# Kernel tuning notes

Hardware: AMD Instinct MI355X
Metric: run time of the kernel (lower is better)

Reference implementation:

```python
import jax, jax.numpy as jnp
import numpy as np

B, NE, NR, D1, D2, L = 64, 40000, 500, 200, 200, 64
BN_EPS = 1e-5


def _batchnorm(x, gamma, beta):
    # training-mode BatchNorm1d: biased batch statistics over axis 0
    mu = jnp.mean(x, axis=0)
    var = jnp.var(x, axis=0)
    return gamma * (x - mu) * jax.lax.rsqrt(var + BN_EPS) + beta


def setup_inputs() -> dict:
    key = jax.random.key(0)
    ks = jax.random.split(key, 10)
    return {
        "e1_idx": jax.random.randint(ks[0], (B,), 0, NE),
        "r_idx": jax.random.randint(ks[1], (B,), 0, NR),
        "E": jax.random.normal(ks[2], (NE, D1), dtype=jnp.float32),
        "R": jax.random.normal(ks[3], (NR, D2), dtype=jnp.float32),
        # W ~ Uniform(-1, 1) as in the torch module
        "W": jax.random.uniform(ks[4], (D2, D1, D1), dtype=jnp.float32, minval=-1.0, maxval=1.0),
        # literals normalized into [0, 1]
        "lits": jax.random.uniform(ks[5], (NE, L), dtype=jnp.float32),
        "c": jax.random.normal(ks[6], (L,), dtype=jnp.float32) * 0.1,
        # variance buffer must be positive
        "var_l": jax.random.uniform(ks[7], (L,), dtype=jnp.float32, minval=0.5, maxval=1.5),
        "nf": jax.random.normal(ks[8], (NR, L), dtype=jnp.float32) * 0.1,
        "bn0_gamma": jnp.ones((D1,), jnp.float32),
        "bn0_beta": jnp.zeros((D1,), jnp.float32),
        "bn1_gamma": jnp.ones((D1,), jnp.float32),
        "bn1_beta": jnp.zeros((D1,), jnp.float32),
    }


def reference(e1_idx, r_idx, E, R, W, lits, c, var_l, nf,
              bn0_gamma, bn0_beta, bn1_gamma, bn1_beta):
    # --- TuckER core ---
    e1 = E[e1_idx]                                   # (B, d1)
    x = _batchnorm(e1, bn0_gamma, bn0_beta)          # (B, d1)
    r = R[r_idx]                                     # (B, d2)
    W_mat = jnp.einsum('bk,kij->bij', r, W)          # (B, d1, d1)
    x = jnp.einsum('bi,bij->bj', x, W_mat)           # (B, d1)
    x = _batchnorm(x, bn1_gamma, bn1_beta)
    score_l = x @ E.T                                # (B, N)

    # --- KBLN numeric-literal branch ---
    n_h = lits[e1_idx]                               # (B, L)
    # broadcast instead of .repeat: (B, 1, L) - (1, N, L) -> (B, N, L)
    n = n_h[:, None, :] - lits[None, :, :]
    phi = jnp.exp(-jnp.square(n - c) / var_l)        # (B, N, L)
    w_nf = nf[r_idx]                                 # (B, L)
    score_n = jnp.einsum('bnl,bl->bn', phi, w_nf)    # (B, N)

    return jax.nn.sigmoid(score_l + score_n)
```

## Files before the change

kernel.cpp:

```cpp
#include <hip/hip_runtime.h>
#include <math.h>

#define BB    64
#define NEC   40000
#define NRC   500
#define D1C   200
#define D2C   200
#define LLC   64
#define BN_EPS 1e-5f
#define LOG2E 1.4426950408889634f

#define WS_XT    0
#define WS_RT    12800
#define WS_TAP   25600
#define WS_WP    29696
#define WS_SL    33792
#define WS_X2BH  33856
#define WS_X2BL  42048
#define WS_Y     50240

typedef short s8v __attribute__((ext_vector_type(8)));
typedef float f4v __attribute__((ext_vector_type(4)));

__device__ __forceinline__ unsigned short bf16_rne(float x) {
  unsigned b = __float_as_uint(x);
  unsigned r = b + 0x7FFFu + ((b >> 16) & 1u);
  return (unsigned short)(r >> 16);
}
__device__ __forceinline__ void split2(float x, unsigned short& h,
                                       unsigned short& l) {
  h = bf16_rne(x);
  float hf = __uint_as_float(((unsigned)h) << 16);
  l = bf16_rne(x - hf);
}

__global__ __launch_bounds__(256) void prep_kernel(
    const int* __restrict__ e1_idx, const int* __restrict__ r_idx,
    const float* __restrict__ E, const float* __restrict__ R,
    const float* __restrict__ lits, const float* __restrict__ c,
    const float* __restrict__ var_l, const float* __restrict__ nf,
    const float* __restrict__ bn0g, const float* __restrict__ bn0b,
    float* __restrict__ ws) {
  float* xT  = ws + WS_XT;
  float* rT  = ws + WS_RT;
  float* taP = ws + WS_TAP;
  float* wP  = ws + WS_WP;
  float* sl  = ws + WS_SL;
  int tid = threadIdx.x;

  if (blockIdx.x == 0) {
    if (tid < D1C) {
      int j = tid;
      float sum = 0.f, sq = 0.f;
      for (int b = 0; b < BB; b++) {
        float e = E[e1_idx[b] * D1C + j];
        sum += e; sq += e * e;
      }
      float mean = sum * (1.f / 64.f);
      float var  = sq  * (1.f / 64.f) - mean * mean;
      float inv  = __builtin_amdgcn_rsqf(var + BN_EPS);
      float g    = bn0g[j] * inv;
      float be   = bn0b[j] - mean * g;
      for (int b = 0; b < BB; b++) {
        xT[j * 64 + b] = g * E[e1_idx[b] * D1C + j] + be;
      }
    }
  } else if (blockIdx.x == 1) {
    for (int idx = tid; idx < D2C * 64; idx += 256) {
      int k = idx >> 6, b = idx & 63;
      rT[idx] = R[r_idx[b] * D2C + k];
    }
  } else if (blockIdx.x == 2) {
    for (int idx = tid; idx < LLC * 64; idx += 256) {
      int l = idx >> 6, b = idx & 63;
      float s = sqrtf(LOG2E / var_l[l]);
      float a = (lits[e1_idx[b] * LLC + l] - c[l]) * s;
      int bp = (b & 15) * 4 + (b >> 4);
      taP[l * 64 + bp] = a + a;
      wP[l * 64 + bp]  = nf[r_idx[b] * LLC + l] * __builtin_amdgcn_exp2f(-a * a);
    }
    if (tid < LLC) sl[tid] = sqrtf(LOG2E / var_l[tid]);
  } else {
    unsigned* z = (unsigned*)(ws + WS_X2BH);
    for (int i = tid; i < 16384; i += 256) z[i] = 0u;
  }
}

__global__ __launch_bounds__(128) void stage1_kernel(
    const float* __restrict__ W, const float* __restrict__ ws_in,
    float* __restrict__ y) {
  const float* xT = ws_in + WS_XT;
  const float* rT = ws_in + WS_RT;
  int k = blockIdx.x, jq = blockIdx.y;
  int lane = threadIdx.x & 63;
  int wid = __builtin_amdgcn_readfirstlane(threadIdx.x >> 6);
  int j0 = jq * 20 + wid * 10;

  float r = rT[k * 64 + lane];
  float acc[10];
#pragma unroll
  for (int jj = 0; jj < 10; jj++) acc[jj] = 0.f;

  const float* Wk = W + (k * D1C) * D1C + j0;
  for (int i = 0; i < D1C; i++) {
    float xv = xT[i * 64 + lane];
    const float* wr = Wk + i * D1C;
#pragma unroll
    for (int jj = 0; jj < 10; jj++) acc[jj] += xv * wr[jj];
  }

  float* yo = y + (k * D1C + j0) * 64 + lane;
#pragma unroll
  for (int jj = 0; jj < 10; jj++) yo[jj * 64] = r * acc[jj];
}

__global__ __launch_bounds__(256) void reduce_bn1_kernel(
    const float* __restrict__ y, const float* __restrict__ bn1g,
    const float* __restrict__ bn1b, float* __restrict__ ws) {
  int j = blockIdx.x;
  int tid = threadIdx.x, b = tid & 63, kq = tid >> 6;

  float s = 0.f;
  const float* yp = y + (kq * 50 * D1C + j) * 64 + b;
  for (int k = 0; k < 50; k++) s += yp[k * D1C * 64];

  __shared__ float part[256];
  part[tid] = s;
  __syncthreads();
  if (tid < 64) {
    float v = part[tid] + part[64 + tid] + part[128 + tid] + part[192 + tid];
    float sum = v, sq = v * v;
#pragma unroll
    for (int o = 32; o > 0; o >>= 1) {
      sum += __shfl_xor(sum, o, 64);
      sq  += __shfl_xor(sq,  o, 64);
    }
    float mean = sum * (1.f / 64.f);
    float var  = sq  * (1.f / 64.f) - mean * mean;
    float inv  = __builtin_amdgcn_rsqf(var + BN_EPS);
    float g    = bn1g[j] * inv;
    float be   = bn1b[j] - mean * g;
    float xv   = g * v + be;
    unsigned short h, l;
    split2(xv, h, l);
    unsigned short* xh = (unsigned short*)(ws + WS_X2BH);
    unsigned short* xl = (unsigned short*)(ws + WS_X2BL);
    xh[tid * 256 + j] = h;
    xl[tid * 256 + j] = l;
  }
}

__global__ __launch_bounds__(256, 2) void final_kernel(
    const float* __restrict__ E, const float* __restrict__ lits,
    const float* __restrict__ ws, float* __restrict__ out) {
  const float* taP = ws + WS_TAP;
  const float* wP  = ws + WS_WP;
  const float* sl  = ws + WS_SL;
  const unsigned short* x2bh = (const unsigned short*)(ws + WS_X2BH);
  const unsigned short* x2bl = (const unsigned short*)(ws + WS_X2BL);

  __shared__ float SM[9216];
  unsigned short* Ah = (unsigned short*)SM;
  unsigned short* Al = Ah + 4608;
  unsigned short* Bh = Ah + 9216;
  unsigned short* Bl = Ah + 13824;

  int n0 = blockIdx.x * 64;
  int tid = threadIdx.x;
  int lane = tid & 63;
  int w = __builtin_amdgcn_readfirstlane(tid >> 6);
  int ln = lane & 15;
  int quad = lane >> 4;

  f4v acc[4];
#pragma unroll
  for (int t = 0; t < 4; t++) acc[t] = (f4v){0.f, 0.f, 0.f, 0.f};

  for (int q = 0; q < 4; q++) {
    int k0 = q * 64;
    __syncthreads();
#pragma unroll
    for (int it = 0; it < 4; it++) {
      int idx = tid + it * 256;
      int row = idx >> 4, c4 = idx & 15, cc = c4 * 4;
      float4 v = make_float4(0.f, 0.f, 0.f, 0.f);
      if (k0 + cc < 200) v = *(const float4*)(E + (n0 + row) * D1C + k0 + cc);
      unsigned short h0, l0, h1, l1, h2, l2, h3, l3;
      split2(v.x, h0, l0); split2(v.y, h1, l1);
      split2(v.z, h2, l2); split2(v.w, h3, l3);
      *(ushort4*)(Ah + row * 72 + cc) = make_ushort4(h0, h1, h2, h3);
      *(ushort4*)(Al + row * 72 + cc) = make_ushort4(l0, l1, l2, l3);
    }
#pragma unroll
    for (int it = 0; it < 4; it++) {
      int idx = tid + it * 256;
      int row = idx >> 4, c4 = idx & 15;
      *(ushort4*)(Bh + row * 72 + c4 * 4) =
          *(const ushort4*)(x2bh + row * 256 + k0 + c4 * 4);
      *(ushort4*)(Bl + row * 72 + c4 * 4) =
          *(const ushort4*)(x2bl + row * 256 + k0 + c4 * 4);
    }
    __syncthreads();

    const unsigned short* Ab  = Ah + (16 * w + ln) * 72 + quad * 8;
    const unsigned short* Alb = Al + (16 * w + ln) * 72 + quad * 8;
#pragma unroll
    for (int ks = 0; ks < 64; ks += 32) {
      s8v ah = *(const s8v*)(Ab + ks);
      s8v al = *(const s8v*)(Alb + ks);
#pragma unroll
      for (int t = 0; t < 4; t++) {
        s8v bh = *(const s8v*)(Bh + (16 * t + ln) * 72 + quad * 8 + ks);
        s8v bl = *(const s8v*)(Bl + (16 * t + ln) * 72 + quad * 8 + ks);
        acc[t] = __builtin_amdgcn_mfma_f32_16x16x32_bf16(ah, bh, acc[t], 0, 0, 0);
        acc[t] = __builtin_amdgcn_mfma_f32_16x16x32_bf16(al, bh, acc[t], 0, 0, 0);
        acc[t] = __builtin_amdgcn_mfma_f32_16x16x32_bf16(ah, bl, acc[t], 0, 0, 0);
      }
    }
  }

  float* Llds = SM;
  float* TAl  = SM + 4352;
  float* Wl   = SM + 6400;
  int nlb = 16 * w + 4 * quad;

  __syncthreads();
#pragma unroll
  for (int it = 0; it < 4; it++) {
    int idx = tid + it * 256;
    int row = idx >> 4, c4 = idx & 15;
    float4 v = *(const float4*)(lits + (n0 + row) * LLC + c4 * 4);
    int l = c4 * 4;
    Llds[(l + 0) * 68 + row] = v.x * sl[l + 0];
    Llds[(l + 1) * 68 + row] = v.y * sl[l + 1];
    Llds[(l + 2) * 68 + row] = v.z * sl[l + 2];
    Llds[(l + 3) * 68 + row] = v.w * sl[l + 3];
  }

  for (int h = 0; h < 2; h++) {
    __syncthreads();
#pragma unroll
    for (int it = 0; it < 2; it++) {
      int idx = tid + it * 256;
      ((float4*)TAl)[idx] = ((const float4*)(taP + h * 2048))[idx];
      ((float4*)Wl)[idx]  = ((const float4*)(wP  + h * 2048))[idx];
    }
    __syncthreads();
    for (int ll = 0; ll < 32; ll++) {
      float4 Lv = *(const float4*)(Llds + (h * 32 + ll) * 68 + nlb);
      float4 ta = *(const float4*)(TAl + ll * 64 + 4 * ln);
      float4 wv = *(const float4*)(Wl  + ll * 64 + 4 * ln);
      float Lc[4]  = {Lv.x, Lv.y, Lv.z, Lv.w};
      float tac[4] = {ta.x, ta.y, ta.z, ta.w};
      float wvc[4] = {wv.x, wv.y, wv.z, wv.w};
      float n2[4];
#pragma unroll
      for (int r = 0; r < 4; r++) n2[r] = -Lc[r] * Lc[r];
#pragma unroll
      for (int t = 0; t < 4; t++) {
#pragma unroll
        for (int r = 0; r < 4; r++) {
          acc[t][r] += wvc[t] *
              __builtin_amdgcn_exp2f(__builtin_fmaf(tac[t], Lc[r], n2[r]));
        }
      }
    }
  }

#pragma unroll
  for (int t = 0; t < 4; t++) {
    float4 o;
    o.x = __builtin_amdgcn_rcpf(1.f + __builtin_amdgcn_exp2f(-LOG2E * acc[t][0]));
    o.y = __builtin_amdgcn_rcpf(1.f + __builtin_amdgcn_exp2f(-LOG2E * acc[t][1]));
    o.z = __builtin_amdgcn_rcpf(1.f + __builtin_amdgcn_exp2f(-LOG2E * acc[t][2]));
    o.w = __builtin_amdgcn_rcpf(1.f + __builtin_amdgcn_exp2f(-LOG2E * acc[t][3]));
    *(float4*)(out + (size_t)(16 * t + ln) * NEC + n0 + nlb) = o;
  }
}

extern "C" void kernel_launch(void* const* d_in, const int* in_sizes, int n_in,
                              void* d_out, int out_size, void* d_ws, size_t ws_size,
                              hipStream_t stream) {
  (void)in_sizes; (void)n_in; (void)out_size; (void)ws_size;
  const int*   e1    = (const int*)d_in[0];
  const int*   ri    = (const int*)d_in[1];
  const float* E     = (const float*)d_in[2];
  const float* R     = (const float*)d_in[3];
  const float* W     = (const float*)d_in[4];
  const float* lits  = (const float*)d_in[5];
  const float* c     = (const float*)d_in[6];
  const float* var_l = (const float*)d_in[7];
  const float* nf    = (const float*)d_in[8];
  const float* bn0g  = (const float*)d_in[9];
  const float* bn0b  = (const float*)d_in[10];
  const float* bn1g  = (const float*)d_in[11];
  const float* bn1b  = (const float*)d_in[12];
  float* out = (float*)d_out;
  float* ws  = (float*)d_ws;
  float* y   = ws + WS_Y;

  prep_kernel<<<4, 256, 0, stream>>>(e1, ri, E, R, lits, c, var_l, nf,
                                     bn0g, bn0b, ws);
  stage1_kernel<<<dim3(200, 10), 128, 0, stream>>>(W, ws, y);
  reduce_bn1_kernel<<<200, 256, 0, stream>>>(y, bn1g, bn1b, ws);
  final_kernel<<<625, 256, 0, stream>>>(E, lits, ws, out);
}
```

Before: 205.8 us.

## Restructure stage1 as register-tiled GEMM with async global-to-LDS double buffering

```diff
diff --git a/kernel.cpp b/kernel.cpp
--- a/kernel.cpp
+++ b/kernel.cpp
@@ -32,6 +32,12 @@
   h = bf16_rne(x);
   float hf = __uint_as_float(((unsigned)h) << 16);
   l = bf16_rne(x - hf);
+}
+
+typedef __attribute__((address_space(1))) const void gvoid_t;
+typedef __attribute__((address_space(3))) void lvoid_t;
+__device__ __forceinline__ void gload_lds16(const float* g, float* l) {
+  __builtin_amdgcn_global_load_lds((gvoid_t*)g, (lvoid_t*)l, 16, 0, 0);
 }
 
 __global__ __launch_bounds__(256) void prep_kernel(
@@ -86,32 +92,79 @@
   }
 }
 
-__global__ __launch_bounds__(128) void stage1_kernel(
+#define S1_STAGE(buf_, s_) do {                                         \
+    int gbase_ = kbase + (s_) * 8000;                                   \
+    _Pragma("unroll")                                                   \
+    for (int r_ = 0; r_ < 4; r_++) {                                    \
+      int off_ = r_ * 2048 + w * 256;                                   \
+      int gi_ = gbase_ + off_ + lane4;                                  \
+      gi_ = gi_ < 7999996 ? gi_ : 7999996;                              \
+      gload_lds16(W + gi_, &Wb[buf_][off_]);                            \
+    }                                                                   \
+  } while (0)
+
+__global__ __launch_bounds__(512) void stage1_kernel(
     const float* __restrict__ W, const float* __restrict__ ws_in,
     float* __restrict__ y) {
   const float* xT = ws_in + WS_XT;
   const float* rT = ws_in + WS_RT;
-  int k = blockIdx.x, jq = blockIdx.y;
-  int lane = threadIdx.x & 63;
-  int wid = __builtin_amdgcn_readfirstlane(threadIdx.x >> 6);
-  int j0 = jq * 20 + wid * 10;
-
-  float r = rT[k * 64 + lane];
-  float acc[10];
-#pragma unroll
-  for (int jj = 0; jj < 10; jj++) acc[jj] = 0.f;
-
-  const float* Wk = W + (k * D1C) * D1C + j0;
-  for (int i = 0; i < D1C; i++) {
-    float xv = xT[i * 64 + lane];
-    const float* wr = Wk + i * D1C;
-#pragma unroll
-    for (int jj = 0; jj < 10; jj++) acc[jj] += xv * wr[jj];
-  }
-
-  float* yo = y + (k * D1C + j0) * 64 + lane;
-#pragma unroll
-  for (int jj = 0; jj < 10; jj++) yo[jj * 64] = r * acc[jj];
+  __shared__ float Wb[2][8192];
+
+  int k = blockIdx.x;
+  int tid = threadIdx.x;
+  int lane = tid & 63;
+  int w = __builtin_amdgcn_readfirstlane(tid >> 6);
+  int jc = w & 3, bh = w >> 2;
+  int j4 = lane & 15, bq = lane >> 4;
+  int j0 = jc * 64 + j4 * 4;
+  int b0 = bh * 32 + bq * 8;
+  bool jok = j0 < 200;
+  int joff = jok ? j0 : 0;
+  int kbase = k * 40000;
+  int lane4 = lane * 4;
+
+  float acc[4][8];
+#pragma unroll
+  for (int jj = 0; jj < 4; jj++)
+#pragma unroll
+    for (int bb = 0; bb < 8; bb++) acc[jj][bb] = 0.f;
+
+  S1_STAGE(0, 0);
+  for (int s = 0; s < 5; s++) {
+    __syncthreads();
+    if (s < 4) S1_STAGE((s + 1) & 1, s + 1);
+    const float* Ws = Wb[s & 1];
+    const float* xrow = xT + s * 40 * 64 + b0;
+#pragma unroll 4
+    for (int ri = 0; ri < 40; ri++) {
+      float4 wv  = *(const float4*)(Ws + ri * 200 + joff);
+      float4 xa  = *(const float4*)(xrow + ri * 64);
+      float4 xb2 = *(const float4*)(xrow + ri * 64 + 4);
+      float wc[4] = {wv.x, wv.y, wv.z, wv.w};
+      float xv[8] = {xa.x, xa.y, xa.z, xa.w, xb2.x, xb2.y, xb2.z, xb2.w};
+#pragma unroll
+      for (int jj = 0; jj < 4; jj++)
+#pragma unroll
+        for (int bb = 0; bb < 8; bb++)
+          acc[jj][bb] += wc[jj] * xv[bb];
+    }
+  }
+
+  if (jok) {
+    float4 r0 = *(const float4*)(rT + k * 64 + b0);
+    float4 r1 = *(const float4*)(rT + k * 64 + b0 + 4);
+    float rv[8] = {r0.x, r0.y, r0.z, r0.w, r1.x, r1.y, r1.z, r1.w};
+#pragma unroll
+    for (int jj = 0; jj < 4; jj++) {
+      float* yo = y + (k * D1C + j0 + jj) * 64 + b0;
+      float4 o0 = make_float4(acc[jj][0] * rv[0], acc[jj][1] * rv[1],
+                              acc[jj][2] * rv[2], acc[jj][3] * rv[3]);
+      float4 o1 = make_float4(acc[jj][4] * rv[4], acc[jj][5] * rv[5],
+                              acc[jj][6] * rv[6], acc[jj][7] * rv[7]);
+      *(float4*)(yo) = o0;
+      *(float4*)(yo + 4) = o1;
+    }
+  }
 }
 
 __global__ __launch_bounds__(256) void reduce_bn1_kernel(
@@ -301,7 +354,7 @@
 
   prep_kernel<<<4, 256, 0, stream>>>(e1, ri, E, R, lits, c, var_l, nf,
                                      bn0g, bn0b, ws);
-  stage1_kernel<<<dim3(200, 10), 128, 0, stream>>>(W, ws, y);
+  stage1_kernel<<<200, 512, 0, stream>>>(W, ws, y);
   reduce_bn1_kernel<<<200, 256, 0, stream>>>(y, bn1g, bn1b, ws);
   final_kernel<<<625, 256, 0, stream>>>(E, lits, ws, out);
 }
```

Result: faster. 199.2 us (-3.2%).
